# Optimization experiments

Measured on AMD Instinct MI355X. Metric: run time of the kernel, lower is better.

Reference implementation:

```python
import jax, jax.numpy as jnp
import numpy as np

T, S, B, H, NH, F = 256, 128, 32, 1024, 16, 4096
D = H // NH  # head dim


def setup_inputs() -> dict:
    key = jax.random.key(0)
    ks = jax.random.split(key, 14)
    w = lambda k, shape: jax.random.normal(k, shape, jnp.float32) * 0.02
    return {
        "x": jax.random.normal(ks[0], (T, B, H), jnp.float32),
        "src_bias": jnp.zeros((B, 1, 1, S), jnp.float32),
        "tgt_bias": jnp.zeros((B, 1, 1, T), jnp.float32),
        "memory": jax.random.normal(ks[1], (S, B, H), jnp.float32),
        # cross-attention projections
        "Wq": w(ks[2], (H, H)), "bq": jnp.zeros((H,), jnp.float32),
        "Wk": w(ks[3], (H, H)), "bk": jnp.zeros((H,), jnp.float32),
        "Wv": w(ks[4], (H, H)), "bv": jnp.zeros((H,), jnp.float32),
        "Wo": w(ks[5], (H, H)), "bo": jnp.zeros((H,), jnp.float32),
        # feed-forward
        "W1": w(ks[6], (H, F)), "b1": jnp.zeros((F,), jnp.float32),
        "W2": w(ks[7], (F, H)), "b2": jnp.zeros((H,), jnp.float32),
        # LSTM gates: input = cat(ffn_x, attn_ctx, h) -> 3H, output 4H (i,j,f,o)
        "Wg": w(ks[8], (3 * H, 4 * H)), "bg": jnp.zeros((4 * H,), jnp.float32),
    }


def _cross_attention(xq, mem, bias, Wq, bq, Wk, bk, Wv, bv, Wo, bo):
    # xq: [B,T,H], mem: [B,S,H], bias: [B,1,1,S]
    b, t, h = xq.shape
    q = (xq @ Wq + bq).reshape(b, t, NH, D) * (D ** -0.5)
    k = (mem @ Wk + bk).reshape(b, -1, NH, D)
    v = (mem @ Wv + bv).reshape(b, -1, NH, D)
    logits = jnp.einsum("bqhd,bkhd->bhqk", q, k) + bias
    wts = jax.nn.softmax(logits, axis=-1)
    ctx = jnp.einsum("bhqk,bkhd->bqhd", wts, v).reshape(b, t, h)
    return ctx @ Wo + bo


def reference(x, src_bias, tgt_bias, memory, Wq, bq, Wk, bk, Wv, bv, Wo, bo,
              W1, b1, W2, b2, Wg, bg):
    # cross attention (time-major -> batch-major -> time-major)
    c_attn = _cross_attention(jnp.transpose(x, (1, 0, 2)),
                              jnp.transpose(memory, (1, 0, 2)),
                              src_bias, Wq, bq, Wk, bk, Wv, bv, Wo, bo)
    c_attn = jnp.transpose(c_attn, (1, 0, 2))  # [T,B,H]

    # feed-forward on x (dropout disabled / eval mode)
    ffn_x = jax.nn.relu(x @ W1 + b1) @ W2 + b2  # [T,B,H]

    xs = jnp.concatenate([ffn_x, c_attn], axis=-1)  # [T,B,2H]
    c0 = jnp.zeros((x.shape[1], H), x.dtype)
    h0 = jnp.zeros((x.shape[1], H), x.dtype)

    def step(carry, xt):
        c, h = carry
        g = jnp.concatenate([xt, h], axis=-1) @ Wg + bg  # [B,4H]
        i = jax.nn.sigmoid(g[:, :H])
        j = jnp.tanh(g[:, H:2 * H])
        f = jax.nn.sigmoid(g[:, 2 * H:3 * H])
        o = jax.nn.sigmoid(g[:, 3 * H:])
        new_c = f * c + i * j
        new_h = o * new_c  # THUMT LSTMCell default activation=None
        return (new_c, new_h), new_h

    (c_f, h_f), hiddens = jax.lax.scan(step, (c0, h0), xs)
    return hiddens, c_f, h_f
```

## Files before the change

### kernel.cpp

```cpp
#include <hip/hip_runtime.h>
#include <cstdint>
#include <cstddef>

#define T_  256
#define S_  128
#define B_  32
#define H_  1024
#define NH_ 16
#define D_  64
#define F_  4096
#define TB_ (T_*B_)
#define SB_ (S_*B_)

typedef unsigned short u16;
typedef unsigned int   u32;
typedef unsigned long long u64;
typedef __attribute__((ext_vector_type(8))) short s16x8;
typedef __attribute__((ext_vector_type(4))) float f32x4;
typedef __attribute__((ext_vector_type(4))) u32  u32x4;

static __device__ __forceinline__ float b2f(u16 u) {
  union { u32 i; float f; } cv; cv.i = ((u32)u) << 16; return cv.f;
}
static __device__ __forceinline__ u16 f2b(float f) {
  union { float f; u32 i; } cv; cv.f = f;
  u32 u = cv.i;
  u32 r = (u + 0x7fffu + ((u >> 16) & 1u)) >> 16;
  return (u16)r;
}
static __device__ __forceinline__ float sigm(float x) {
  return 1.0f / (1.0f + __expf(-x));
}
static __device__ __forceinline__ float tanh_fast(float x) {
  float e2 = __expf(2.0f * x);
  return 1.0f - 2.0f / (e2 + 1.0f);
}

typedef const __attribute__((address_space(1))) void* gvoidp;
typedef __attribute__((address_space(3))) void* lvoidp;
static __device__ __forceinline__ void gl_lds16(const void* g, void* l) {
  __builtin_amdgcn_global_load_lds((gvoidp)g, (lvoidp)l, 16, 0, 0);
}

static __device__ __forceinline__ void cast_task(const float* __restrict__ in,
                                                 u16* __restrict__ out, int lb, int tid) {
  int i = lb * 256 + tid;
  float4 v = reinterpret_cast<const float4*>(in)[i];
  ushort4 o;
  o.x = f2b(v.x); o.y = f2b(v.y); o.z = f2b(v.z); o.w = f2b(v.w);
  reinterpret_cast<ushort4*>(out)[i] = o;
}

static __device__ __forceinline__ void tr32(const float* __restrict__ in,
                                            u16* __restrict__ out,
                                            int R, int C, int lin, int tid,
                                            float tile[32][33]) {
  const int gx = C >> 5;
  const int bx = lin % gx, by = lin / gx;
  const int c0 = bx << 5, r0 = by << 5;
  const int tx = tid & 31, ty = tid >> 5;
  #pragma unroll
  for (int k = 0; k < 32; k += 8)
    tile[ty + k][tx] = in[(size_t)(r0 + ty + k) * C + c0 + tx];
  __syncthreads();
  #pragma unroll
  for (int k = 0; k < 32; k += 8)
    out[(size_t)(c0 + ty + k) * R + r0 + tx] = f2b(tile[tx][ty + k]);
}

#define NB_SENT 1
#define NB_CX   8192
#define NB_CM   4096
#define NB_TSQ  1024
#define NB_TW1  4096
#define NB_TW2  4096
#define NB_TGX  8192
#define NB_TWH  4096
#define NB_PREP (NB_SENT + NB_CX + NB_CM + 4*NB_TSQ + NB_TW1 + NB_TW2 + NB_TGX + NB_TWH)

__global__ __launch_bounds__(256) void prep_all(
    const float* __restrict__ x, const float* __restrict__ mem,
    const float* __restrict__ Wq, const float* __restrict__ Wk,
    const float* __restrict__ Wv, const float* __restrict__ Wo,
    const float* __restrict__ W1, const float* __restrict__ W2,
    const float* __restrict__ Wg,
    u16* __restrict__ xb, u16* __restrict__ memb,
    u16* __restrict__ WqT, u16* __restrict__ WkT, u16* __restrict__ WvT,
    u16* __restrict__ WoT, u16* __restrict__ W1T, u16* __restrict__ W2T,
    u16* __restrict__ WgxT, u16* __restrict__ WhT, u32* __restrict__ sent)
{
  __shared__ float tile[32][33];
  int b = blockIdx.x;
  const int tid = threadIdx.x;
  if (b < NB_SENT) { sent[tid] = 0; sent[tid + 256] = 0; return; }
  b -= NB_SENT;
  if (b < NB_CX) { cast_task(x, xb, b, tid); return; }      b -= NB_CX;
  if (b < NB_CM) { cast_task(mem, memb, b, tid); return; }  b -= NB_CM;
  if (b < NB_TSQ) { tr32(Wq, WqT, H_, H_, b, tid, tile); return; }  b -= NB_TSQ;
  if (b < NB_TSQ) { tr32(Wk, WkT, H_, H_, b, tid, tile); return; }  b -= NB_TSQ;
  if (b < NB_TSQ) { tr32(Wv, WvT, H_, H_, b, tid, tile); return; }  b -= NB_TSQ;
  if (b < NB_TSQ) { tr32(Wo, WoT, H_, H_, b, tid, tile); return; }  b -= NB_TSQ;
  if (b < NB_TW1) { tr32(W1, W1T, H_, F_, b, tid, tile); return; }  b -= NB_TW1;
  if (b < NB_TW2) { tr32(W2, W2T, F_, H_, b, tid, tile); return; }  b -= NB_TW2;
  if (b < NB_TGX) { tr32(Wg, WgxT, 2 * H_, 4 * H_, b, tid, tile); return; } b -= NB_TGX;
  tr32(Wg + (size_t)(2 * H_) * (4 * H_), WhT, H_, 4 * H_, b, tid, tile);
}

#define SBAR      asm volatile("s_barrier" ::: "memory")
#define VMCNT4    asm volatile("s_waitcnt vmcnt(4)" ::: "memory")
#define VMCNT0    asm volatile("s_waitcnt vmcnt(0)" ::: "memory")

struct GJob {
  const u16* A; const u16* Bt; u16* Out; const float* bias;
  int Kdim; int ostride; int relu; int gridx; int nblk; float scale;
};
struct GBatch { GJob j[4]; int starts[4]; int njobs; };

static __device__ __forceinline__ void stage_region(
    const u16* __restrict__ src, int Kdim, int row0,
    int kt, int kh, char* lds_region, int tid) {
  const int w  = tid >> 6;
  const int r  = tid >> 2;
  const int cs = (tid & 3) ^ ((tid >> 3) & 3);
  const int kbase = kt * 64 + kh * 32 + cs * 8;
  gl_lds16(src + (size_t)(row0 + r) * Kdim + kbase,        lds_region + w * 1024);
  gl_lds16(src + (size_t)(row0 + 128 + r) * Kdim + kbase,  lds_region + 8192 + w * 1024);
}

static __device__ __forceinline__ s16x8 ldsf(const char* sm, int base, int row, int quad) {
  return *(const s16x8*)(sm + base + row * 64 + ((quad ^ ((row >> 1) & 3)) << 4));
}

__global__ __launch_bounds__(512, 2) void gemm256(GBatch gb)
{
  __shared__ __align__(16) u16 smem[65536];
  char* sm = (char*)smem;
  const int bid = blockIdx.x;
  int ji = 0;
  #pragma unroll
  for (int t = 1; t < 4; t++)
    if (t < gb.njobs && bid >= gb.starts[t]) ji = t;
  const GJob J = gb.j[ji];
  const int lin = bid - gb.starts[ji];
  const int wg = (lin & 7) * (J.nblk >> 3) + (lin >> 3);
  const int bx = wg % J.gridx, by = wg / J.gridx;
  const int bm = by << 8, bn = bx << 8;

  const int tid = threadIdx.x;
  const int wavei = tid >> 6, lane = tid & 63;
  const int quad = lane >> 4, l16 = lane & 15;
  const int wm = wavei >> 2, wn = wavei & 3;
  const int NT = J.Kdim >> 6;
  const int arow = wm * 128;
  const int brow = wn * 64;

  f32x4 acc[8][4] = {};

  stage_region(J.A,  J.Kdim, bm, 0, 0, sm + 0,     tid);
  stage_region(J.Bt, J.Kdim, bn, 0, 0, sm + 32768, tid);
  stage_region(J.A,  J.Kdim, bm, 0, 1, sm + 16384, tid);
  stage_region(J.Bt, J.Kdim, bn, 0, 1, sm + 49152, tid);
  VMCNT4;
  SBAR;

  for (int kt = 0; kt < NT; kt++) {
    const int p = (kt & 1) << 16;
    const int q = p ^ 65536;
    const int Ab = p, Bb = p + 32768;
    const bool st = (kt + 1 < NT);
    s16x8 af[8], b0, b1;

    #pragma unroll
    for (int mi = 0; mi < 8; mi++)
      af[mi] = ldsf(sm, Ab, arow + mi * 16 + l16, quad);
    b0 = ldsf(sm, Bb, brow + l16, quad);
    b1 = ldsf(sm, Bb, brow + 16 + l16, quad);
    if (st) stage_region(J.A, J.Kdim, bm, kt + 1, 0, sm + q, tid);
    SBAR;
    __builtin_amdgcn_s_setprio(1);
    #pragma unroll
    for (int mi = 0; mi < 8; mi++) {
      acc[mi][0] = __builtin_amdgcn_mfma_f32_16x16x32_bf16(af[mi], b0, acc[mi][0], 0, 0, 0);
      acc[mi][1] = __builtin_amdgcn_mfma_f32_16x16x32_bf16(af[mi], b1, acc[mi][1], 0, 0, 0);
    }
    __builtin_amdgcn_s_setprio(0);
    SBAR;

    b0 = ldsf(sm, Bb, brow + 32 + l16, quad);
    b1 = ldsf(sm, Bb, brow + 48 + l16, quad);
    if (st) stage_region(J.Bt, J.Kdim, bn, kt + 1, 0, sm + q + 32768, tid);
    SBAR;
    __builtin_amdgcn_s_setprio(1);
    #pragma unroll
    for (int mi = 0; mi < 8; mi++) {
      acc[mi][2] = __builtin_amdgcn_mfma_f32_16x16x32_bf16(af[mi], b0, acc[mi][2], 0, 0, 0);
      acc[mi][3] = __builtin_amdgcn_mfma_f32_16x16x32_bf16(af[mi], b1, acc[mi][3], 0, 0, 0);
    }
    __builtin_amdgcn_s_setprio(0);
    if (st) { VMCNT4; } else { VMCNT0; }
    SBAR;

    const int Ab1 = Ab + 16384, Bb1 = Bb + 16384;
    #pragma unroll
    for (int mi = 0; mi < 8; mi++)
      af[mi] = ldsf(sm, Ab1, arow + mi * 16 + l16, quad);
    b0 = ldsf(sm, Bb1, brow + l16, quad);
    b1 = ldsf(sm, Bb1, brow + 16 + l16, quad);
    if (st) stage_region(J.A, J.Kdim, bm, kt + 1, 1, sm + q + 16384, tid);
    SBAR;
    __builtin_amdgcn_s_setprio(1);
    #pragma unroll
    for (int mi = 0; mi < 8; mi++) {
      acc[mi][0] = __builtin_amdgcn_mfma_f32_16x16x32_bf16(af[mi], b0, acc[mi][0], 0, 0, 0);
      acc[mi][1] = __builtin_amdgcn_mfma_f32_16x16x32_bf16(af[mi], b1, acc[mi][1], 0, 0, 0);
    }
    __builtin_amdgcn_s_setprio(0);
    SBAR;

    b0 = ldsf(sm, Bb1, brow + 32 + l16, quad);
    b1 = ldsf(sm, Bb1, brow + 48 + l16, quad);
    if (st) stage_region(J.Bt, J.Kdim, bn, kt + 1, 1, sm + q + 49152, tid);
    SBAR;
    __builtin_amdgcn_s_setprio(1);
    #pragma unroll
    for (int mi = 0; mi < 8; mi++) {
      acc[mi][2] = __builtin_amdgcn_mfma_f32_16x16x32_bf16(af[mi], b0, acc[mi][2], 0, 0, 0);
      acc[mi][3] = __builtin_amdgcn_mfma_f32_16x16x32_bf16(af[mi], b1, acc[mi][3], 0, 0, 0);
    }
    __builtin_amdgcn_s_setprio(0);
    if (st) { VMCNT4; }
    SBAR;
  }

  #pragma unroll
  for (int mi = 0; mi < 8; mi++) {
    #pragma unroll
    for (int nj = 0; nj < 4; nj++) {
      const int colo = bn + wn * 64 + nj * 16 + l16;
      const float bv = J.bias[colo];
      #pragma unroll
      for (int r = 0; r < 4; r++) {
        const int rowo = bm + wm * 128 + mi * 16 + quad * 4 + r;
        float vv = (acc[mi][nj][r] + bv) * J.scale;
        if (J.relu) vv = fmaxf(vv, 0.0f);
        J.Out[(size_t)rowo * J.ostride + colo] = f2b(vv);
      }
    }
  }
}

__global__ __launch_bounds__(256) void attn_kernel(
    const u16* __restrict__ q, const u16* __restrict__ k, const u16* __restrict__ v,
    const float* __restrict__ src_bias, u16* __restrict__ ctx)
{
  __shared__ u16 ks[S_ * D_];
  __shared__ u16 vs[S_ * D_];
  const int b  = blockIdx.x >> 4;
  const int nh = blockIdx.x & 15;
  const int tid = threadIdx.x;

  for (int i = tid; i < (S_ * D_) / 8; i += 256) {
    int s = i >> 3, c = (i & 7) * 8;
    *(uint4*)&ks[s * D_ + c] = *(const uint4*)&k[((size_t)(s * B_ + b)) * H_ + nh * D_ + c];
    *(uint4*)&vs[s * D_ + c] = *(const uint4*)&v[((size_t)(s * B_ + b)) * H_ + nh * D_ + c];
  }
  __syncthreads();

  const int t = tid;
  float qf[D_];
  const u16* qp = &q[((size_t)(t * B_ + b)) * H_ + nh * D_];
  #pragma unroll
  for (int c8 = 0; c8 < D_; c8 += 8) {
    uint4 qv = *(const uint4*)&qp[c8];
    const u16* pu = (const u16*)&qv;
    #pragma unroll
    for (int j = 0; j < 8; j++) qf[c8 + j] = b2f(pu[j]);
  }
  const float* bias = src_bias + b * S_;

  float m = -1e30f, l = 0.0f;
  float of[D_] = {};
  for (int s = 0; s < S_; s++) {
    float dot = 0.0f;
    #pragma unroll
    for (int d = 0; d < D_; d++) dot += qf[d] * b2f(ks[s * D_ + d]);
    dot += bias[s];
    if (dot > m + 8.0f) {
      const float sc = __expf(m - dot);
      l *= sc;
      #pragma unroll
      for (int d = 0; d < D_; d++) of[d] *= sc;
      m = dot;
    }
    const float w = __expf(dot - m);
    l += w;
    #pragma unroll
    for (int d = 0; d < D_; d++) of[d] += w * b2f(vs[s * D_ + d]);
  }
  const float inv = 1.0f / l;
  u16* op = &ctx[((size_t)(t * B_ + b)) * H_ + nh * D_];
  #pragma unroll
  for (int c8 = 0; c8 < D_; c8 += 8) {
    u16 tmp[8];
    #pragma unroll
    for (int j = 0; j < 8; j++) tmp[j] = f2b(of[c8 + j] * inv);
    *(uint4*)&op[c8] = *(const uint4*)tmp;
  }
}

#define ISSUE2(K) { \
  const u16* b0_ = hb + ((size_t)(wave * 16 + (K) * 2 + (quad >> 1))) * 512 + \
                   (quad & 1) * 8 + l16 * 16; \
  asm volatile("global_load_dwordx4 %0, %1, off sc0 sc1" : "=v"(ba[K][0]) : "v"(b0_) : "memory"); \
  asm volatile("global_load_dwordx4 %0, %1, off sc0 sc1" : "=v"(ba[K][1]) : "v"(b0_ + 256) : "memory"); }

#define DO_MFMA(A0,A1,KC)                                                           \
  { _Pragma("unroll") for (int g_ = 0; g_ < 3; g_++) {                              \
      s16x8 wf_ = *(const s16x8*)&Wl[wave][((g_ * 8 + (KC)) * 64 + lane) * 8];      \
      acc[g_][0] = __builtin_amdgcn_mfma_f32_16x16x32_bf16(A0, wf_, acc[g_][0], 0, 0, 0); \
      acc[g_][1] = __builtin_amdgcn_mfma_f32_16x16x32_bf16(A1, wf_, acc[g_][1], 0, 0, 0); } \
    acc[3][0] = __builtin_amdgcn_mfma_f32_16x16x32_bf16(A0, wo[KC], acc[3][0], 0, 0, 0);  \
    acc[3][1] = __builtin_amdgcn_mfma_f32_16x16x32_bf16(A1, wo[KC], acc[3][1], 0, 0, 0); }

#define CONSUME(K, NSTR) { \
  asm volatile("s_waitcnt vmcnt(" NSTR ")" ::: "memory"); \
  __builtin_amdgcn_sched_barrier(0); \
  DO_MFMA(ba[K][0], ba[K][1], K); }

__global__ __launch_bounds__(256, 1) void lstm_persistent(
    const u16* __restrict__ g_x, const u16* __restrict__ WhT,
    u16* __restrict__ hb16, u32* __restrict__ sent, float* __restrict__ out)
{
  __shared__ __align__(16) u16 Wl[4][3 * 8 * 64 * 8];
  __shared__ float P[4][4][32][17];
  const int bk = blockIdx.x, tid = threadIdx.x;
  const int wave = tid >> 6, lane = tid & 63;
  const int quad = lane >> 4, l16 = lane & 15;

  for (int i = lane; i < 3 * 8 * 64; i += 64) {
    const int g  = (i >> 9) & 3;
    const int kc = (i >> 6) & 7;
    const int row = g * H_ + bk * 16 + (lane & 15);
    const int col = wave * 256 + kc * 32 + (lane >> 4) * 8;
    *(uint4*)&Wl[wave][i * 8] = *(const uint4*)&WhT[(size_t)row * H_ + col];
  }
  s16x8 wo[8];
  {
    const int row = 3 * H_ + bk * 16 + (lane & 15);
    const int colb = wave * 256 + (lane >> 4) * 8;
    #pragma unroll
    for (int kc = 0; kc < 8; kc++)
      wo[kc] = *(const s16x8*)&WhT[(size_t)row * H_ + colb + kc * 32];
  }
  __syncthreads();

  const int pb = tid >> 4, pc = tid & 15;
  const int col = bk * 16 + pc;
  float creg[2] = {0.0f, 0.0f};

  float gxp[2][4];
  #pragma unroll
  for (int ii = 0; ii < 2; ii++)
    #pragma unroll
    for (int g = 0; g < 4; g++)
      gxp[ii][g] = b2f(g_x[((size_t)(pb + ii * 16)) * (4 * H_) + g * H_ + col]);

  s16x8 ba[8][2];

  for (int t = 0; t < T_; t++) {
    if (t > 0) {
      const u32 st = (u32)t;
      const u16* hb = hb16 + ((t & 1) ^ 1) * 32768;

      { const u32* sp = sent + ((size_t)(((t & 1) ^ 1) * 256 + wave * 64 + lane));
        u32 sv;
        do {
          asm volatile("global_load_dword %0, %1, off sc0 sc1\n\ts_waitcnt vmcnt(0)"
                       : "=v"(sv) : "v"(sp) : "memory");
        } while (!__all(sv == st)); }

      f32x4 acc[4][2] = {};
      ISSUE2(0) ISSUE2(1) ISSUE2(2) ISSUE2(3)
      ISSUE2(4) ISSUE2(5) ISSUE2(6) ISSUE2(7)
      CONSUME(0, "14") CONSUME(1, "12") CONSUME(2, "10") CONSUME(3, "8")
      CONSUME(4, "6")  CONSUME(5, "4")  CONSUME(6, "2")  CONSUME(7, "0")

      #pragma unroll
      for (int g = 0; g < 4; g++)
        #pragma unroll
        for (int mt = 0; mt < 2; mt++)
          #pragma unroll
          for (int r = 0; r < 4; r++)
            P[wave][g][mt * 16 + quad * 4 + r][l16] = acc[g][mt][r];
    }
    __syncthreads();

    float gs[2][4];
    #pragma unroll
    for (int ii = 0; ii < 2; ii++) {
      const int b_ = pb + ii * 16;
      #pragma unroll
      for (int g = 0; g < 4; g++) {
        float s = gxp[ii][g];
        if (t > 0) s += P[0][g][b_][pc] + P[1][g][b_][pc] + P[2][g][b_][pc] + P[3][g][b_][pc];
        gs[ii][g] = s;
      }
    }
    __syncthreads();

    float hn[2], cn[2];
    #pragma unroll
    for (int ii = 0; ii < 2; ii++) {
      const float iv = sigm(gs[ii][0]);
      const float jv = tanh_fast(gs[ii][1]);
      const float fv = sigm(gs[ii][2]);
      const float ov = sigm(gs[ii][3]);
      cn[ii] = fv * creg[ii] + iv * jv;
      hn[ii] = ov * cn[ii];
      creg[ii] = cn[ii];
    }

    {
      u32 lo0 = f2b(hn[0]), lo1 = f2b(hn[1]);
      u32 hi0 = __shfl_down(lo0, 1), hi1 = __shfl_down(lo1, 1);
      if ((pc & 1) == 0) {
        u32* hw32 = (u32*)(hb16 + (t & 1) * 32768);
        u32 dw0 = lo0 | (hi0 << 16);
        u32 dw1 = lo1 | (hi1 << 16);
        __hip_atomic_store(&hw32[(size_t)bk * 256 + pb * 8 + (pc >> 1)], dw0,
                           __ATOMIC_RELAXED, __HIP_MEMORY_SCOPE_AGENT);
        __hip_atomic_store(&hw32[(size_t)bk * 256 + (pb + 16) * 8 + (pc >> 1)], dw1,
                           __ATOMIC_RELAXED, __HIP_MEMORY_SCOPE_AGENT);
      }
      asm volatile("s_waitcnt vmcnt(0)" ::: "memory");
      if (lane == 0)
        __hip_atomic_store(&sent[(size_t)(t & 1) * 256 + bk * 4 + wave], (u32)(t + 1),
                           __ATOMIC_RELAXED, __HIP_MEMORY_SCOPE_AGENT);
    }

    #pragma unroll
    for (int ii = 0; ii < 2; ii++) {
      const int b_ = pb + ii * 16;
      out[(size_t)t * (B_ * H_) + b_ * H_ + col] = hn[ii];
      if (t == T_ - 1) {
        out[(size_t)T_ * B_ * H_ + b_ * H_ + col] = cn[ii];
        out[(size_t)T_ * B_ * H_ + B_ * H_ + b_ * H_ + col] = hn[ii];
      }
    }
    if (t < T_ - 1) {
      #pragma unroll
      for (int ii = 0; ii < 2; ii++)
        #pragma unroll
        for (int g = 0; g < 4; g++)
          gxp[ii][g] = b2f(g_x[((size_t)(t + 1) * B_ + pb + ii * 16) * (4 * H_) + g * H_ + col]);
    }
  }
}

extern "C" void kernel_launch(void* const* d_in, const int* in_sizes, int n_in,
                              void* d_out, int out_size, void* d_ws, size_t ws_size,
                              hipStream_t stream)
{
  const float* x        = (const float*)d_in[0];
  const float* src_bias = (const float*)d_in[1];
  const float* mem      = (const float*)d_in[3];
  const float* Wq = (const float*)d_in[4];  const float* bq = (const float*)d_in[5];
  const float* Wk = (const float*)d_in[6];  const float* bk = (const float*)d_in[7];
  const float* Wv = (const float*)d_in[8];  const float* bv = (const float*)d_in[9];
  const float* Wo = (const float*)d_in[10]; const float* bo = (const float*)d_in[11];
  const float* W1 = (const float*)d_in[12]; const float* b1f = (const float*)d_in[13];
  const float* W2 = (const float*)d_in[14]; const float* b2f_ = (const float*)d_in[15];
  const float* Wg = (const float*)d_in[16]; const float* bg = (const float*)d_in[17];
  float* out = (float*)d_out;

  char* p = (char*)d_ws;
  u16* xb   = (u16*)p; p += (size_t)TB_ * H_ * 2;
  u16* memb = (u16*)p; p += (size_t)SB_ * H_ * 2;
  u16* WqT  = (u16*)p; p += (size_t)H_ * H_ * 2;
  u16* WkT  = (u16*)p; p += (size_t)H_ * H_ * 2;
  u16* WvT  = (u16*)p; p += (size_t)H_ * H_ * 2;
  u16* WoT  = (u16*)p; p += (size_t)H_ * H_ * 2;
  u16* W1T  = (u16*)p; p += (size_t)F_ * H_ * 2;
  u16* W2T  = (u16*)p; p += (size_t)H_ * F_ * 2;
  u16* WgxT = (u16*)p; p += (size_t)(4 * H_) * (2 * H_) * 2;
  u16* WhT  = (u16*)p; p += (size_t)(4 * H_) * H_ * 2;
  u16* qb   = (u16*)p; p += (size_t)TB_ * H_ * 2;
  u16* kb   = (u16*)p; p += (size_t)SB_ * H_ * 2;
  u16* vb   = (u16*)p; p += (size_t)SB_ * H_ * 2;
  u16* ctxb = (u16*)p; p += (size_t)TB_ * H_ * 2;
  u16* xs   = (u16*)p; p += (size_t)TB_ * (2 * H_) * 2;
  u16* h1   = (u16*)p; p += (size_t)TB_ * F_ * 2;
  u16* hb16 = (u16*)p; p += (size_t)2 * 32768 * 2;
  u32* sent = (u32*)p; p += (size_t)2 * 256 * 4;
  u16* gx   = h1;

  prep_all<<<dim3(NB_PREP), dim3(256), 0, stream>>>(
      x, mem, Wq, Wk, Wv, Wo, W1, W2, Wg,
      xb, memb, WqT, WkT, WvT, WoT, W1T, W2T, WgxT, WhT, sent);

  GBatch gb1 = {};
  gb1.j[0] = { xb,   WqT, qb, bq,  H_, H_, 0, H_ / 256, (TB_ / 256) * (H_ / 256), 0.125f };
  gb1.j[1] = { memb, WkT, kb, bk,  H_, H_, 0, H_ / 256, (SB_ / 256) * (H_ / 256), 1.0f   };
  gb1.j[2] = { memb, WvT, vb, bv,  H_, H_, 0, H_ / 256, (SB_ / 256) * (H_ / 256), 1.0f   };
  gb1.j[3] = { xb,   W1T, h1, b1f, H_, F_, 1, F_ / 256, (TB_ / 256) * (F_ / 256), 1.0f   };
  gb1.starts[0] = 0;
  gb1.starts[1] = gb1.j[0].nblk;
  gb1.starts[2] = gb1.starts[1] + gb1.j[1].nblk;
  gb1.starts[3] = gb1.starts[2] + gb1.j[2].nblk;
  gb1.njobs = 4;
  const int nb1 = gb1.starts[3] + gb1.j[3].nblk;
  gemm256<<<dim3(nb1), dim3(512), 0, stream>>>(gb1);

  attn_kernel<<<dim3(B_ * NH_), dim3(256), 0, stream>>>(qb, kb, vb, src_bias, ctxb);

  GBatch gb2 = {};
  gb2.j[0] = { ctxb, WoT, xs + H_, bo,   H_, 2 * H_, 0, H_ / 256, (TB_ / 256) * (H_ / 256), 1.0f };
  gb2.j[1] = { h1,   W2T, xs,      b2f_, F_, 2 * H_, 0, H_ / 256, (TB_ / 256) * (H_ / 256), 1.0f };
  gb2.starts[0] = 0;
  gb2.starts[1] = gb2.j[0].nblk;
  gb2.njobs = 2;
  const int nb2 = gb2.starts[1] + gb2.j[1].nblk;
  gemm256<<<dim3(nb2), dim3(512), 0, stream>>>(gb2);

  GBatch gb3 = {};
  gb3.j[0] = { xs, WgxT, gx, bg, 2 * H_, 4 * H_, 0, 4 * H_ / 256, (TB_ / 256) * (4 * H_ / 256), 1.0f };
  gb3.starts[0] = 0;
  gb3.njobs = 1;
  gemm256<<<dim3(gb3.j[0].nblk), dim3(512), 0, stream>>>(gb3);

  lstm_persistent<<<dim3(64), dim3(256), 0, stream>>>(gx, WhT, hb16, sent, out);
}
```

Measured before the change: 1.523 ms.

## Move late weight transposes into attention kernel launch to overlap work

Weight transposes for Wo, W2 and Wg, which are only needed by later GEMMs, are moved out of the prep kernel and into extra blocks of the attention kernel. This shortens the prep stage in front of the first GEMM batch and fills idle compute units while the 512 attention blocks run. The merged kernel now allocates 32KB of shared memory per block, which may reduce occupancy for the transpose blocks.

```diff
diff --git a/kernel.cpp b/kernel.cpp
--- a/kernel.cpp
+++ b/kernel.cpp
@@ -54,7 +54,7 @@
 static __device__ __forceinline__ void tr32(const float* __restrict__ in,
                                             u16* __restrict__ out,
                                             int R, int C, int lin, int tid,
-                                            float tile[32][33]) {
+                                            float (*tile)[33]) {
   const int gx = C >> 5;
   const int bx = lin % gx, by = lin / gx;
   const int c0 = bx << 5, r0 = by << 5;
@@ -73,21 +73,15 @@
 #define NB_CM   4096
 #define NB_TSQ  1024
 #define NB_TW1  4096
-#define NB_TW2  4096
-#define NB_TGX  8192
-#define NB_TWH  4096
-#define NB_PREP (NB_SENT + NB_CX + NB_CM + 4*NB_TSQ + NB_TW1 + NB_TW2 + NB_TGX + NB_TWH)
+#define NB_PREP (NB_SENT + NB_CX + NB_CM + 3*NB_TSQ + NB_TW1)
 
 __global__ __launch_bounds__(256) void prep_all(
     const float* __restrict__ x, const float* __restrict__ mem,
     const float* __restrict__ Wq, const float* __restrict__ Wk,
-    const float* __restrict__ Wv, const float* __restrict__ Wo,
-    const float* __restrict__ W1, const float* __restrict__ W2,
-    const float* __restrict__ Wg,
+    const float* __restrict__ Wv, const float* __restrict__ W1,
     u16* __restrict__ xb, u16* __restrict__ memb,
     u16* __restrict__ WqT, u16* __restrict__ WkT, u16* __restrict__ WvT,
-    u16* __restrict__ WoT, u16* __restrict__ W1T, u16* __restrict__ W2T,
-    u16* __restrict__ WgxT, u16* __restrict__ WhT, u32* __restrict__ sent)
+    u16* __restrict__ W1T, u32* __restrict__ sent)
 {
   __shared__ float tile[32][33];
   int b = blockIdx.x;
@@ -99,11 +93,7 @@
   if (b < NB_TSQ) { tr32(Wq, WqT, H_, H_, b, tid, tile); return; }  b -= NB_TSQ;
   if (b < NB_TSQ) { tr32(Wk, WkT, H_, H_, b, tid, tile); return; }  b -= NB_TSQ;
   if (b < NB_TSQ) { tr32(Wv, WvT, H_, H_, b, tid, tile); return; }  b -= NB_TSQ;
-  if (b < NB_TSQ) { tr32(Wo, WoT, H_, H_, b, tid, tile); return; }  b -= NB_TSQ;
-  if (b < NB_TW1) { tr32(W1, W1T, H_, F_, b, tid, tile); return; }  b -= NB_TW1;
-  if (b < NB_TW2) { tr32(W2, W2T, F_, H_, b, tid, tile); return; }  b -= NB_TW2;
-  if (b < NB_TGX) { tr32(Wg, WgxT, 2 * H_, 4 * H_, b, tid, tile); return; } b -= NB_TGX;
-  tr32(Wg + (size_t)(2 * H_) * (4 * H_), WhT, H_, 4 * H_, b, tid, tile);
+  tr32(W1, W1T, H_, F_, b, tid, tile);
 }
 
 #define SBAR      asm volatile("s_barrier" ::: "memory")
@@ -249,15 +239,41 @@
   }
 }
 
-__global__ __launch_bounds__(256) void attn_kernel(
+#define NB_ATTN  512
+#define NB_TWO2  1024
+#define NB_TW22  4096
+#define NB_TGX2  8192
+#define NB_TWH2  4096
+#define NB_ATTNL (NB_ATTN + NB_TWO2 + NB_TW22 + NB_TGX2 + NB_TWH2)
+
+__global__ __launch_bounds__(256) void attn_prep(
     const u16* __restrict__ q, const u16* __restrict__ k, const u16* __restrict__ v,
-    const float* __restrict__ src_bias, u16* __restrict__ ctx)
+    const float* __restrict__ src_bias, u16* __restrict__ ctx,
+    const float* __restrict__ Wo, const float* __restrict__ W2,
+    const float* __restrict__ Wg,
+    u16* __restrict__ WoT, u16* __restrict__ W2T,
+    u16* __restrict__ WgxT, u16* __restrict__ WhT)
 {
-  __shared__ u16 ks[S_ * D_];
-  __shared__ u16 vs[S_ * D_];
+  __shared__ __align__(16) char shraw[32768];
+  const int tid = threadIdx.x;
+
+  if (blockIdx.x >= NB_ATTN) {
+    float (*tile)[33] = (float(*)[33])shraw;
+    int tix = blockIdx.x - NB_ATTN;
+    if (tix < NB_TWO2) { tr32(Wo, WoT, H_, H_, tix, tid, tile); return; }
+    tix -= NB_TWO2;
+    if (tix < NB_TW22) { tr32(W2, W2T, F_, H_, tix, tid, tile); return; }
+    tix -= NB_TW22;
+    if (tix < NB_TGX2) { tr32(Wg, WgxT, 2 * H_, 4 * H_, tix, tid, tile); return; }
+    tix -= NB_TGX2;
+    tr32(Wg + (size_t)(2 * H_) * (4 * H_), WhT, H_, 4 * H_, tix, tid, tile);
+    return;
+  }
+
+  u16* ks = (u16*)shraw;
+  u16* vs = ks + S_ * D_;
   const int b  = blockIdx.x >> 4;
   const int nh = blockIdx.x & 15;
-  const int tid = threadIdx.x;
 
   for (int i = tid; i < (S_ * D_) / 8; i += 256) {
     int s = i >> 3, c = (i & 7) * 8;
@@ -495,8 +511,7 @@
   u16* gx   = h1;
 
   prep_all<<<dim3(NB_PREP), dim3(256), 0, stream>>>(
-      x, mem, Wq, Wk, Wv, Wo, W1, W2, Wg,
-      xb, memb, WqT, WkT, WvT, WoT, W1T, W2T, WgxT, WhT, sent);
+      x, mem, Wq, Wk, Wv, W1, xb, memb, WqT, WkT, WvT, W1T, sent);
 
   GBatch gb1 = {};
   gb1.j[0] = { xb,   WqT, qb, bq,  H_, H_, 0, H_ / 256, (TB_ / 256) * (H_ / 256), 0.125f };
@@ -511,7 +526,8 @@
   const int nb1 = gb1.starts[3] + gb1.j[3].nblk;
   gemm256<<<dim3(nb1), dim3(512), 0, stream>>>(gb1);
 
-  attn_kernel<<<dim3(B_ * NH_), dim3(256), 0, stream>>>(qb, kb, vb, src_bias, ctxb);
+  attn_prep<<<dim3(NB_ATTNL), dim3(256), 0, stream>>>(
+      qb, kb, vb, src_bias, ctxb, Wo, W2, Wg, WoT, W2T, WgxT, WhT);
 
   GBatch gb2 = {};
   gb2.j[0] = { ctxb, WoT, xs + H_, bo,   H_, 2 * H_, 0, H_ / 256, (TB_ / 256) * (H_ / 256), 1.0f };
```

New measurement: 1.492 ms. 1.02x faster.
